# Kernel tuning notes

Hardware: AMD Instinct MI355X
Metric: run time of the kernel (lower is better)

The kernel has to match this reference:

```python
import jax, jax.numpy as jnp
import numpy as np

B, T, D = 2, 2048, 1024
H, DK, DV = 16, 64, 64
FF = 4096
EPS = 1e-6


def layer_norm(x, gamma, beta):
    mu = jnp.mean(x, axis=-1, keepdims=True)
    var = jnp.var(x, axis=-1, keepdims=True)
    return (x - mu) * jax.lax.rsqrt(var + EPS) * gamma + beta


def setup_inputs() -> dict:
    key = jax.random.key(0)
    ks = jax.random.split(key, 16)
    s = 0.02
    return {
        "inputs": jax.random.normal(ks[0], (B, T, D), jnp.float32),
        "Wq": jax.random.normal(ks[1], (D, H, DK), jnp.float32) * s,
        "Wk": jax.random.normal(ks[2], (D, H, DK), jnp.float32) * s,
        "Wv": jax.random.normal(ks[3], (D, H, DV), jnp.float32) * s,
        "Wo": jax.random.normal(ks[4], (D, H, DV), jnp.float32) * s,
        "W1": jax.random.normal(ks[5], (D, FF), jnp.float32) * s,
        "b1": jnp.zeros((FF,), jnp.float32),
        "W2": jax.random.normal(ks[6], (FF, D), jnp.float32) * s,
        "b2": jnp.zeros((D,), jnp.float32),
        "g1": jnp.ones((D,), jnp.float32),
        "be1": jnp.zeros((D,), jnp.float32),
        "g2": jnp.ones((D,), jnp.float32),
        "be2": jnp.zeros((D,), jnp.float32),
    }


def reference(inputs, Wq, Wk, Wv, Wo, W1, b1, W2, b2, g1, be1, g2, be2):
    x = inputs
    scale = 1.0 / jnp.sqrt(jnp.asarray(DK, x.dtype))
    q = jnp.einsum("btd,dhk->bthk", x, Wq) * scale
    k = jnp.einsum("bsd,dhk->bshk", x, Wk)
    v = jnp.einsum("bsd,dhv->bshv", x, Wv)
    # [B,H,T,S] attention scores; causal mask (t >= s)
    score = jnp.einsum("bshk,bthk->bhts", k, q)
    causal = jnp.tril(jnp.ones((T, T), bool))  # [T,S]
    score = jnp.where(causal[None, None], score, jnp.finfo(score.dtype).min)
    attn = jax.nn.softmax(score, axis=-1)
    ctx = jnp.einsum("bhts,bshv->bthv", attn, v)
    attn_out = jnp.einsum("bthv,dhv->btd", ctx, Wo)
    h = layer_norm(x + attn_out, g1, be1)
    ffn = jnp.maximum(h @ W1 + b1, 0.0) @ W2 + b2
    return layer_norm(h + ffn, g2, be2)
```

## Files before the change

### kernel.cpp

```cpp
#include <hip/hip_runtime.h>
#include <math.h>

#define T_SEQ 2048
#define D_MODEL 1024
#define NHEAD 16
#define DHEAD 64
#define FF_DIM 4096
#define NTOK 4096
#define LN_EPS 1e-6f

typedef unsigned short u16;
typedef __attribute__((ext_vector_type(8))) __bf16 bf16x8;
typedef __attribute__((ext_vector_type(4))) float f32x4;

typedef const void __attribute__((address_space(1))) gvoid;
typedef void __attribute__((address_space(3))) lvoid;

__device__ __forceinline__ u16 f2bf(float f) {
  unsigned u = __float_as_uint(f);
  return (u16)((u + 0x7fffu + ((u >> 16) & 1u)) >> 16);
}
__device__ __forceinline__ float bf2f(u16 u) {
  return __uint_as_float((unsigned)u << 16);
}

__device__ __forceinline__ void gll16(const u16* g, u16* l) {
  __builtin_amdgcn_global_load_lds((gvoid*)g, (lvoid*)l, 16, 0, 0);
}

__device__ __forceinline__ bf16x8 lds_frag(const u16* lds, int row, int chunk) {
  return *(const bf16x8*)&lds[row * 64 + ((chunk ^ (row & 7)) * 8)];
}

__global__ __launch_bounds__(256) void conv_f2b(const float* __restrict__ in,
                                                u16* __restrict__ out, int n) {
  const int i = (blockIdx.x * 256 + threadIdx.x) * 4;
  if (i >= n) return;
  const float4 v = *(const float4*)&in[i];
  ushort4 o;
  o.x = f2bf(v.x); o.y = f2bf(v.y); o.z = f2bf(v.z); o.w = f2bf(v.w);
  *(ushort4*)&out[i] = o;
}

__global__ __launch_bounds__(256) void transpose_f2b(
    const float* __restrict__ in, u16* __restrict__ out, int K, int N,
    float scale) {
  __shared__ u16 t[64][72];
  const int tid = threadIdx.x;
  const int k0 = blockIdx.y * 64, n0 = blockIdx.x * 64;
  const int nl = tid & 63;
#pragma unroll
  for (int i = 0; i < 16; ++i) {
    const int kl = (tid >> 6) * 16 + i;
    t[nl][kl] = f2bf(in[(size_t)(k0 + kl) * N + n0 + nl] * scale);
  }
  __syncthreads();
  const int nr = tid >> 2, kc = (tid & 3) * 16;
  const uint4 a = *(const uint4*)&t[nr][kc];
  const uint4 b = *(const uint4*)&t[nr][kc + 8];
  *(uint4*)&out[(size_t)(n0 + nr) * K + k0 + kc] = a;
  *(uint4*)&out[(size_t)(n0 + nr) * K + k0 + kc + 8] = b;
}

__global__ __launch_bounds__(256) void transpose_v(const u16* __restrict__ vin,
                                                   u16* __restrict__ vout) {
  __shared__ u16 t[64][72];
  const int tid = threadIdx.x;
  const int bh = blockIdx.y;
  const int t0 = blockIdx.x * 64;
  const u16* src = vin + ((size_t)bh * T_SEQ + t0) * 64;
#pragma unroll
  for (int i = 0; i < 2; ++i) {
    const int r = i * 32 + (tid >> 3);
    const int ch = tid & 7;
    *(uint4*)&t[r][ch * 8] = *(const uint4*)&src[(size_t)r * 64 + ch * 8];
  }
  __syncthreads();
  const int d = tid >> 2, p = (tid & 3) * 16;
  alignas(16) u16 tmp[16];
#pragma unroll
  for (int i = 0; i < 16; ++i) tmp[i] = t[p + i][d];
  u16* dst = vout + ((size_t)bh * 64 + d) * T_SEQ + t0 + p;
  *(uint4*)&dst[0] = *(const uint4*)&tmp[0];
  *(uint4*)&dst[8] = *(const uint4*)&tmp[8];
}

template <int OUTMODE, bool BIAS, bool RELU>
__global__ __launch_bounds__(256) void gemm_mfma(
    const u16* __restrict__ A, const u16* __restrict__ BT,
    const float* __restrict__ bias, void* __restrict__ C,
    int M, int N, int K, float scale) {
  __shared__ u16 smem[16384];

  const int tid = threadIdx.x;
  const int w = tid >> 6, lane = tid & 63;

  const int nwg = gridDim.x * gridDim.y;
  int bid = blockIdx.y * gridDim.x + blockIdx.x;
  const int cpx = nwg >> 3;
  bid = (bid & 7) * cpx + (bid >> 3);
  const int bx = bid % gridDim.x, by = bid / gridDim.x;
  const int m0 = by * 128, n0 = bx * 128;
  const int wr = (w >> 1) * 64, wc = (w & 1) * 64;

  f32x4 acc[4][4];
#pragma unroll
  for (int i = 0; i < 4; ++i)
#pragma unroll
    for (int j = 0; j < 4; ++j) acc[i][j] = (f32x4)0.f;

  const int srow = w * 32 + (lane >> 2);
  const int scol = (lane & 3) * 8;
  const u16* gA0 = A + (size_t)(m0 + srow) * K + scol;
  const u16* gA1 = gA0 + (size_t)16 * K;
  const u16* gB0 = BT + (size_t)(n0 + srow) * K + scol;
  const u16* gB1 = gB0 + (size_t)16 * K;

  const int arow = lane & 15;
  const int koff = (lane >> 4) * 8;

  auto stage = [&](int buf, int k0) {
    u16* base = smem + buf * 8192;
    gll16(gA0 + k0, base + w * 1024);
    gll16(gA1 + k0, base + w * 1024 + 512);
    gll16(gB0 + k0, base + 4096 + w * 1024);
    gll16(gB1 + k0, base + 4096 + w * 1024 + 512);
  };

  stage(0, 0);
  __syncthreads();

  const int nk = K >> 5;
  for (int it = 0; it < nk; ++it) {
    const int buf = it & 1;
    if (it + 1 < nk) stage(buf ^ 1, (it + 1) << 5);

    const u16* sb = smem + buf * 8192;
    bf16x8 af[4], bff[4];
#pragma unroll
    for (int m = 0; m < 4; ++m)
      af[m] = *(const bf16x8*)&sb[(wr + m * 16 + arow) * 32 + koff];
#pragma unroll
    for (int n = 0; n < 4; ++n)
      bff[n] = *(const bf16x8*)&sb[4096 + (wc + n * 16 + arow) * 32 + koff];
#pragma unroll
    for (int m = 0; m < 4; ++m)
#pragma unroll
      for (int n = 0; n < 4; ++n)
        acc[m][n] = __builtin_amdgcn_mfma_f32_16x16x32_bf16(
            af[m], bff[n], acc[m][n], 0, 0, 0);
    __syncthreads();
  }

  const int rbase = (lane >> 4) * 4;
  const int cl = lane & 15;
#pragma unroll
  for (int n = 0; n < 4; ++n) {
    const int col = n0 + wc + n * 16 + cl;
    const float bia = BIAS ? bias[col] : 0.f;
#pragma unroll
    for (int m = 0; m < 4; ++m) {
      const int row0 = m0 + wr + m * 16 + rbase;
#pragma unroll
      for (int r = 0; r < 4; ++r) {
        float vv = acc[m][n][r] * scale + bia;
        if (RELU) vv = fmaxf(vv, 0.f);
        const int row = row0 + r;
        if (OUTMODE == 1) {
          ((u16*)C)[(size_t)row * N + col] = f2bf(vv);
        } else {
          const int reg = col >> 10, cl2 = col & 1023;
          const size_t off =
              (size_t)reg * 4194304 +
              ((size_t)((row >> 11) * NHEAD + (cl2 >> 6)) * T_SEQ +
               (row & 2047)) * 64 + (cl2 & 63);
          ((u16*)C)[off] = f2bf(vv);
        }
      }
    }
  }
}

__global__ __launch_bounds__(256) void attn_mfma(
    const u16* __restrict__ qg, const u16* __restrict__ kg,
    const u16* __restrict__ vtg, u16* __restrict__ ctx) {
  __shared__ u16 Ks[2][64 * 64];
  __shared__ u16 Vs[2][64 * 64];
  __shared__ u16 Ps[4][32 * 64];

  const int tid = threadIdx.x;
  const int w = tid >> 6, lane = tid & 63;
  const int qt = gridDim.x - 1 - blockIdx.x;
  const int bh = blockIdx.y;
  const int lo = lane & 15, hi = lane >> 4;
  const int r8 = lane >> 3, cswz = (lane & 7) ^ r8;

  const u16* qhead = qg + (size_t)bh * (T_SEQ * 64);
  const u16* khead = kg + (size_t)bh * (T_SEQ * 64);
  const u16* vhead = vtg + (size_t)bh * (64 * T_SEQ);

  const int qbase = qt * 128;
  const int q0w = qbase + w * 32;
  bf16x8 qa[2][2];
#pragma unroll
  for (int u = 0; u < 2; ++u) {
    const u16* qr = &qhead[(size_t)(q0w + u * 16 + lo) * 64];
    qa[u][0] = *(const bf16x8*)&qr[hi * 8];
    qa[u][1] = *(const bf16x8*)&qr[32 + hi * 8];
  }

  f32x4 o[2][4];
#pragma unroll
  for (int u = 0; u < 2; ++u)
#pragma unroll
    for (int dt = 0; dt < 4; ++dt) o[u][dt] = (f32x4)0.f;
  float mrow[2][4], lrow[2][4];
#pragma unroll
  for (int u = 0; u < 2; ++u)
#pragma unroll
    for (int r = 0; r < 4; ++r) { mrow[u][r] = -INFINITY; lrow[u][r] = 0.f; }

  const int nt = 2 * qt + 2;

  auto stage = [&](int buf, int s0) {
#pragma unroll
    for (int i = 0; i < 2; ++i) {
      const int row = w * 16 + i * 8 + r8;
      gll16(khead + (size_t)(s0 + row) * 64 + cswz * 8,
            &Ks[buf][(w * 16 + i * 8) * 64]);
      gll16(vhead + (size_t)row * T_SEQ + s0 + cswz * 8,
            &Vs[buf][(w * 16 + i * 8) * 64]);
    }
  };

  stage(0, 0);
  __syncthreads();

  for (int it = 0; it < nt; ++it) {
    const int buf = it & 1;
    if (it + 1 < nt) stage(buf ^ 1, (it + 1) * 64);

    const bool lastT = (it == nt - 1), diagT = (it == nt - 2);
    if (!(lastT && w < 2)) {
      f32x4 s[2][4];
      __builtin_amdgcn_s_setprio(1);
#pragma unroll
      for (int c = 0; c < 4; ++c) {
        const bf16x8 kb0 = lds_frag(Ks[buf], c * 16 + lo, hi);
        const bf16x8 kb1 = lds_frag(Ks[buf], c * 16 + lo, 4 + hi);
#pragma unroll
        for (int u = 0; u < 2; ++u) {
          f32x4 a = (f32x4)0.f;
          a = __builtin_amdgcn_mfma_f32_16x16x32_bf16(qa[u][0], kb0, a, 0, 0, 0);
          a = __builtin_amdgcn_mfma_f32_16x16x32_bf16(qa[u][1], kb1, a, 0, 0, 0);
          s[u][c] = a;
        }
      }
      __builtin_amdgcn_s_setprio(0);

      if ((diagT && w < 2) || (lastT && w >= 2)) {
#pragma unroll
        for (int c = 0; c < 4; ++c) {
          const int sg = c * 16 + lo;
#pragma unroll
          for (int u = 0; u < 2; ++u)
#pragma unroll
            for (int r = 0; r < 4; ++r) {
              const int rl = (w * 32 + u * 16 + hi * 4 + r) & 63;
              if (sg > rl) s[u][c][r] = -1e30f;
            }
        }
      }

      float mx[2][4];
      bool myok = true;
#pragma unroll
      for (int u = 0; u < 2; ++u)
#pragma unroll
        for (int r = 0; r < 4; ++r) {
          float m4 = fmaxf(fmaxf(s[u][0][r], s[u][1][r]),
                           fmaxf(s[u][2][r], s[u][3][r]));
          m4 = fmaxf(m4, __shfl_xor(m4, 1));
          m4 = fmaxf(m4, __shfl_xor(m4, 2));
          m4 = fmaxf(m4, __shfl_xor(m4, 4));
          m4 = fmaxf(m4, __shfl_xor(m4, 8));
          mx[u][r] = m4;
          myok = myok && (m4 <= mrow[u][r] + 11.5f);
        }
      float corr[2][4];
#pragma unroll
      for (int u = 0; u < 2; ++u)
#pragma unroll
        for (int r = 0; r < 4; ++r) corr[u][r] = 1.f;
      if (!__all(myok)) {
#pragma unroll
        for (int u = 0; u < 2; ++u)
#pragma unroll
          for (int r = 0; r < 4; ++r) {
            const float mn = fmaxf(mrow[u][r], mx[u][r]);
            corr[u][r] = exp2f(mrow[u][r] - mn);
            mrow[u][r] = mn;
          }
#pragma unroll
        for (int u = 0; u < 2; ++u)
#pragma unroll
          for (int dt = 0; dt < 4; ++dt)
#pragma unroll
            for (int r = 0; r < 4; ++r) o[u][dt][r] *= corr[u][r];
      }
      float pr[2][4][4];
#pragma unroll
      for (int u = 0; u < 2; ++u)
#pragma unroll
        for (int r = 0; r < 4; ++r) {
          float ps = 0.f;
#pragma unroll
          for (int c = 0; c < 4; ++c) {
            pr[u][c][r] = exp2f(s[u][c][r] - mrow[u][r]);
            ps += pr[u][c][r];
          }
          ps += __shfl_xor(ps, 1);
          ps += __shfl_xor(ps, 2);
          ps += __shfl_xor(ps, 4);
          ps += __shfl_xor(ps, 8);
          lrow[u][r] = lrow[u][r] * corr[u][r] + ps;
        }

      u16* pw = &Ps[w][0];
#pragma unroll
      for (int c = 0; c < 4; ++c) {
        const int schunk = c * 2 + (lo >> 3);
        const int sb = lo & 7;
#pragma unroll
        for (int u = 0; u < 2; ++u)
#pragma unroll
          for (int r = 0; r < 4; ++r) {
            const int rw = u * 16 + hi * 4 + r;
            pw[rw * 64 + ((schunk ^ (rw & 7)) * 8) + sb] = f2bf(pr[u][c][r]);
          }
      }
      bf16x8 pa[2][2];
#pragma unroll
      for (int u = 0; u < 2; ++u) {
        pa[u][0] = lds_frag(pw, u * 16 + lo, hi);
        pa[u][1] = lds_frag(pw, u * 16 + lo, 4 + hi);
      }

      __builtin_amdgcn_s_setprio(1);
#pragma unroll
      for (int dt = 0; dt < 4; ++dt) {
        const bf16x8 vb0 = lds_frag(Vs[buf], dt * 16 + lo, hi);
        const bf16x8 vb1 = lds_frag(Vs[buf], dt * 16 + lo, 4 + hi);
#pragma unroll
        for (int u = 0; u < 2; ++u) {
          o[u][dt] = __builtin_amdgcn_mfma_f32_16x16x32_bf16(pa[u][0], vb0,
                                                             o[u][dt], 0, 0, 0);
          o[u][dt] = __builtin_amdgcn_mfma_f32_16x16x32_bf16(pa[u][1], vb1,
                                                             o[u][dt], 0, 0, 0);
        }
      }
      __builtin_amdgcn_s_setprio(0);
    }
    __syncthreads();
  }

  const int b = bh >> 4, h = bh & 15;
#pragma unroll
  for (int u = 0; u < 2; ++u)
#pragma unroll
    for (int r = 0; r < 4; ++r) {
      const float inv = 1.0f / lrow[u][r];
      const int t = qbase + w * 32 + u * 16 + hi * 4 + r;
      u16* dst = ctx + ((size_t)(b * T_SEQ + t) * NHEAD + h) * 64;
#pragma unroll
      for (int dt = 0; dt < 4; ++dt)
        dst[dt * 16 + lo] = f2bf(o[u][dt][r] * inv);
    }
}

template <bool EMIT_BF>
__global__ __launch_bounds__(256) void add_layernorm(
    const float* __restrict__ x, const u16* __restrict__ y,
    const float* __restrict__ g, const float* __restrict__ be,
    float* __restrict__ out, u16* __restrict__ out_bf) {
  const int row = blockIdx.x;
  const int tid = threadIdx.x;
  const size_t base = (size_t)row * D_MODEL + tid * 4;

  const float4 xv = *(const float4*)&x[base];
  const ushort4 yv = *(const ushort4*)&y[base];
  const float v0 = xv.x + bf2f(yv.x), v1 = xv.y + bf2f(yv.y);
  const float v2 = xv.z + bf2f(yv.z), v3 = xv.w + bf2f(yv.w);

  float s = v0 + v1 + v2 + v3;
  float ss = v0 * v0 + v1 * v1 + v2 * v2 + v3 * v3;
#pragma unroll
  for (int off = 32; off > 0; off >>= 1) {
    s += __shfl_down(s, off);
    ss += __shfl_down(ss, off);
  }
  __shared__ float red[8];
  const int wid = tid >> 6, lane = tid & 63;
  if (lane == 0) { red[wid] = s; red[4 + wid] = ss; }
  __syncthreads();
  s = red[0] + red[1] + red[2] + red[3];
  ss = red[4] + red[5] + red[6] + red[7];

  const float mean = s * (1.0f / D_MODEL);
  const float var = ss * (1.0f / D_MODEL) - mean * mean;
  const float rr = rsqrtf(var + LN_EPS);

  const float4 g4 = *(const float4*)&g[tid * 4];
  const float4 b4 = *(const float4*)&be[tid * 4];
  float4 o4;
  o4.x = (v0 - mean) * rr * g4.x + b4.x;
  o4.y = (v1 - mean) * rr * g4.y + b4.y;
  o4.z = (v2 - mean) * rr * g4.z + b4.z;
  o4.w = (v3 - mean) * rr * g4.w + b4.w;
  *(float4*)&out[base] = o4;
  if (EMIT_BF) {
    ushort4 ob;
    ob.x = f2bf(o4.x); ob.y = f2bf(o4.y); ob.z = f2bf(o4.z); ob.w = f2bf(o4.w);
    *(ushort4*)&out_bf[base] = ob;
  }
}

extern "C" void kernel_launch(void* const* d_in, const int* in_sizes, int n_in,
                              void* d_out, int out_size, void* d_ws,
                              size_t ws_size, hipStream_t stream) {
  const float* x  = (const float*)d_in[0];
  const float* Wq = (const float*)d_in[1];
  const float* Wk = (const float*)d_in[2];
  const float* Wv = (const float*)d_in[3];
  const float* Wo = (const float*)d_in[4];
  const float* W1 = (const float*)d_in[5];
  const float* b1 = (const float*)d_in[6];
  const float* W2 = (const float*)d_in[7];
  const float* b2 = (const float*)d_in[8];
  const float* g1 = (const float*)d_in[9];
  const float* be1 = (const float*)d_in[10];
  const float* g2 = (const float*)d_in[11];
  const float* be2 = (const float*)d_in[12];

  char* ws = (char*)d_ws;
  const size_t MB = 1u << 20;
  u16*   x_bf    = (u16*)(ws + 0 * MB);
  u16*   WqkvT   = (u16*)(ws + 8 * MB);
  u16*   WoB     = (u16*)(ws + 14 * MB);
  u16*   W1T     = (u16*)(ws + 16 * MB);
  u16*   W2T     = (u16*)(ws + 24 * MB);
  u16*   q_bf    = (u16*)(ws + 32 * MB);
  u16*   v_bf    = (u16*)(ws + 48 * MB);
  u16*   vT_bf   = (u16*)(ws + 56 * MB);
  u16*   ctx_bf  = (u16*)(ws + 64 * MB);
  u16*   attn_bf = (u16*)(ws + 72 * MB);
  float* h       = (float*)(ws + 80 * MB);
  u16*   h_bf    = (u16*)(ws + 0 * MB);
  u16*   ffn1_bf = (u16*)(ws + 32 * MB);
  u16*   ffn2_bf = (u16*)(ws + 8 * MB);

  const dim3 blk(256);
  const float lg2e = 1.44269504f;

  conv_f2b<<<NTOK, blk, 0, stream>>>(x, x_bf, NTOK * D_MODEL);
  transpose_f2b<<<dim3(16, 16), blk, 0, stream>>>(Wq, WqkvT, D_MODEL, D_MODEL,
                                                  0.125f * lg2e);
  transpose_f2b<<<dim3(16, 16), blk, 0, stream>>>(Wk, WqkvT + 1024 * 1024,
                                                  D_MODEL, D_MODEL, 1.f);
  transpose_f2b<<<dim3(16, 16), blk, 0, stream>>>(Wv, WqkvT + 2 * 1024 * 1024,
                                                  D_MODEL, D_MODEL, 1.f);
  conv_f2b<<<1024, blk, 0, stream>>>(Wo, WoB, D_MODEL * D_MODEL);
  transpose_f2b<<<dim3(64, 16), blk, 0, stream>>>(W1, W1T, D_MODEL, FF_DIM, 1.f);
  transpose_f2b<<<dim3(16, 64), blk, 0, stream>>>(W2, W2T, FF_DIM, D_MODEL, 1.f);

  gemm_mfma<2, false, false><<<dim3(24, 32), blk, 0, stream>>>(
      x_bf, WqkvT, nullptr, q_bf, NTOK, 3072, D_MODEL, 1.f);

  transpose_v<<<dim3(32, 32), blk, 0, stream>>>(v_bf, vT_bf);

  attn_mfma<<<dim3(T_SEQ / 128, 32), blk, 0, stream>>>(q_bf, q_bf + 4194304,
                                                       vT_bf, ctx_bf);

  gemm_mfma<1, false, false><<<dim3(8, 32), blk, 0, stream>>>(
      ctx_bf, WoB, nullptr, attn_bf, NTOK, D_MODEL, D_MODEL, 1.f);

  add_layernorm<true><<<NTOK, blk, 0, stream>>>(x, attn_bf, g1, be1, h, h_bf);

  gemm_mfma<1, true, true><<<dim3(32, 32), blk, 0, stream>>>(
      h_bf, W1T, b1, ffn1_bf, NTOK, FF_DIM, D_MODEL, 1.f);
  gemm_mfma<1, true, false><<<dim3(8, 32), blk, 0, stream>>>(
      ffn1_bf, W2T, b2, ffn2_bf, NTOK, D_MODEL, FF_DIM, 1.f);

  add_layernorm<false><<<NTOK, blk, 0, stream>>>(h, ffn2_bf, g2, be2,
                                                 (float*)d_out, nullptr);
}
```

Before: 447.0 us.

## Rewrite attention with 32x32 MFMA, transposed scores and in-register P

The attention kernel now computes S^T = K·Q^T with 32x32x16 MFMAs, so each lane owns one query row. Row max and sum then need only one cross-half shuffle, and the softmax state is a single scalar per lane. P is packed to bf16 with v_cvt_pk_bf16_f32 and rearranged with v_permlane32_swap, so it feeds the PV MFMA directly and the LDS round-trip for P is gone. The output goes through an LDS staging buffer (reusing Ks) so the context store is coalesced in 16-byte writes. The cost is larger accumulator register footprint and inline asm that ties the kernel to gfx950 instructions.

```diff
diff --git a/kernel.cpp b/kernel.cpp
--- a/kernel.cpp
+++ b/kernel.cpp
@@ -10,8 +10,10 @@
 #define LN_EPS 1e-6f
 
 typedef unsigned short u16;
+typedef unsigned int u32;
 typedef __attribute__((ext_vector_type(8))) __bf16 bf16x8;
 typedef __attribute__((ext_vector_type(4))) float f32x4;
+typedef __attribute__((ext_vector_type(16))) float f32x16;
 
 typedef const void __attribute__((address_space(1))) gvoid;
 typedef void __attribute__((address_space(3))) lvoid;
@@ -23,6 +25,11 @@
 __device__ __forceinline__ float bf2f(u16 u) {
   return __uint_as_float((unsigned)u << 16);
 }
+__device__ __forceinline__ u32 cvtpk(float lo, float hi) {
+  u32 r;
+  asm("v_cvt_pk_bf16_f32 %0, %1, %2" : "=v"(r) : "v"(lo), "v"(hi));
+  return r;
+}
 
 __device__ __forceinline__ void gll16(const u16* g, u16* l) {
   __builtin_amdgcn_global_load_lds((gvoid*)g, (lvoid*)l, 16, 0, 0);
@@ -31,6 +38,8 @@
 __device__ __forceinline__ bf16x8 lds_frag(const u16* lds, int row, int chunk) {
   return *(const bf16x8*)&lds[row * 64 + ((chunk ^ (row & 7)) * 8)];
 }
+
+union BF8 { u32 u[4]; bf16x8 v; };
 
 __global__ __launch_bounds__(256) void conv_f2b(const float* __restrict__ in,
                                                 u16* __restrict__ out, int n) {
@@ -186,13 +195,12 @@
     const u16* __restrict__ vtg, u16* __restrict__ ctx) {
   __shared__ u16 Ks[2][64 * 64];
   __shared__ u16 Vs[2][64 * 64];
-  __shared__ u16 Ps[4][32 * 64];
 
   const int tid = threadIdx.x;
   const int w = tid >> 6, lane = tid & 63;
   const int qt = gridDim.x - 1 - blockIdx.x;
   const int bh = blockIdx.y;
-  const int lo = lane & 15, hi = lane >> 4;
+  const int l31 = lane & 31, hi32 = lane >> 5;
   const int r8 = lane >> 3, cswz = (lane & 7) ^ r8;
 
   const u16* qhead = qg + (size_t)bh * (T_SEQ * 64);
@@ -200,25 +208,15 @@
   const u16* vhead = vtg + (size_t)bh * (64 * T_SEQ);
 
   const int qbase = qt * 128;
-  const int q0w = qbase + w * 32;
-  bf16x8 qa[2][2];
-#pragma unroll
-  for (int u = 0; u < 2; ++u) {
-    const u16* qr = &qhead[(size_t)(q0w + u * 16 + lo) * 64];
-    qa[u][0] = *(const bf16x8*)&qr[hi * 8];
-    qa[u][1] = *(const bf16x8*)&qr[32 + hi * 8];
-  }
-
-  f32x4 o[2][4];
-#pragma unroll
-  for (int u = 0; u < 2; ++u)
-#pragma unroll
-    for (int dt = 0; dt < 4; ++dt) o[u][dt] = (f32x4)0.f;
-  float mrow[2][4], lrow[2][4];
-#pragma unroll
-  for (int u = 0; u < 2; ++u)
-#pragma unroll
-    for (int r = 0; r < 4; ++r) { mrow[u][r] = -INFINITY; lrow[u][r] = 0.f; }
+  const int qrow = qbase + w * 32 + l31;
+
+  bf16x8 qb[4];
+#pragma unroll
+  for (int ks2 = 0; ks2 < 4; ++ks2)
+    qb[ks2] = *(const bf16x8*)&qhead[(size_t)qrow * 64 + ks2 * 16 + hi32 * 8];
+
+  f32x16 o0 = (f32x16)0.f, o1 = (f32x16)0.f;
+  float m = -INFINITY, l = 0.f;
 
   const int nt = 2 * qt + 2;
 
@@ -242,140 +240,125 @@
 
     const bool lastT = (it == nt - 1), diagT = (it == nt - 2);
     if (!(lastT && w < 2)) {
-      f32x4 s[2][4];
+      f32x16 st0 = (f32x16)0.f, st1 = (f32x16)0.f;
       __builtin_amdgcn_s_setprio(1);
 #pragma unroll
-      for (int c = 0; c < 4; ++c) {
-        const bf16x8 kb0 = lds_frag(Ks[buf], c * 16 + lo, hi);
-        const bf16x8 kb1 = lds_frag(Ks[buf], c * 16 + lo, 4 + hi);
-#pragma unroll
-        for (int u = 0; u < 2; ++u) {
-          f32x4 a = (f32x4)0.f;
-          a = __builtin_amdgcn_mfma_f32_16x16x32_bf16(qa[u][0], kb0, a, 0, 0, 0);
-          a = __builtin_amdgcn_mfma_f32_16x16x32_bf16(qa[u][1], kb1, a, 0, 0, 0);
-          s[u][c] = a;
+      for (int ks2 = 0; ks2 < 4; ++ks2) {
+        const bf16x8 kf0 = lds_frag(Ks[buf], l31, ks2 * 2 + hi32);
+        st0 = __builtin_amdgcn_mfma_f32_32x32x16_bf16(kf0, qb[ks2], st0, 0, 0, 0);
+      }
+#pragma unroll
+      for (int ks2 = 0; ks2 < 4; ++ks2) {
+        const bf16x8 kf1 = lds_frag(Ks[buf], 32 + l31, ks2 * 2 + hi32);
+        st1 = __builtin_amdgcn_mfma_f32_32x32x16_bf16(kf1, qb[ks2], st1, 0, 0, 0);
+      }
+      __builtin_amdgcn_s_setprio(0);
+
+      if ((diagT && w < 2) || (lastT && w >= 2)) {
+        const int s0g = it * 64;
+#pragma unroll
+        for (int r = 0; r < 16; ++r) {
+          const int rowm = (r & 3) + 8 * (r >> 2) + 4 * hi32;
+          if (s0g + rowm > qrow) st0[r] = -1e30f;
+          if (s0g + 32 + rowm > qrow) st1[r] = -1e30f;
         }
       }
-      __builtin_amdgcn_s_setprio(0);
-
-      if ((diagT && w < 2) || (lastT && w >= 2)) {
-#pragma unroll
-        for (int c = 0; c < 4; ++c) {
-          const int sg = c * 16 + lo;
-#pragma unroll
-          for (int u = 0; u < 2; ++u)
-#pragma unroll
-            for (int r = 0; r < 4; ++r) {
-              const int rl = (w * 32 + u * 16 + hi * 4 + r) & 63;
-              if (sg > rl) s[u][c][r] = -1e30f;
-            }
+
+      float mx = fmaxf(st0[0], st1[0]);
+#pragma unroll
+      for (int r = 1; r < 16; ++r) mx = fmaxf(mx, fmaxf(st0[r], st1[r]));
+      mx = fmaxf(mx, __shfl_xor(mx, 32));
+
+      float corr = 1.f;
+      if (!__all(mx <= m + 11.5f)) {
+        const float mn = fmaxf(m, mx);
+        corr = exp2f(m - mn);
+        m = mn;
+#pragma unroll
+        for (int r = 0; r < 16; ++r) { o0[r] *= corr; o1[r] *= corr; }
+      }
+      float ps = 0.f;
+#pragma unroll
+      for (int r = 0; r < 16; ++r) {
+        st0[r] = exp2f(st0[r] - m);
+        st1[r] = exp2f(st1[r] - m);
+        ps += st0[r] + st1[r];
+      }
+      ps += __shfl_xor(ps, 32);
+      l = l * corr + ps;
+
+      BF8 pb[4];
+#pragma unroll
+      for (int blk = 0; blk < 2; ++blk) {
+        {
+          u32 x0 = cvtpk(st0[blk * 8 + 0], st0[blk * 8 + 1]);
+          u32 x1 = cvtpk(st0[blk * 8 + 2], st0[blk * 8 + 3]);
+          u32 y0 = cvtpk(st0[blk * 8 + 4], st0[blk * 8 + 5]);
+          u32 y1 = cvtpk(st0[blk * 8 + 6], st0[blk * 8 + 7]);
+          asm("v_permlane32_swap_b32 %0, %1" : "+v"(x0), "+v"(y0));
+          asm("v_permlane32_swap_b32 %0, %1" : "+v"(x1), "+v"(y1));
+          pb[blk].u[0] = x0; pb[blk].u[1] = x1;
+          pb[blk].u[2] = y0; pb[blk].u[3] = y1;
         }
-      }
-
-      float mx[2][4];
-      bool myok = true;
-#pragma unroll
-      for (int u = 0; u < 2; ++u)
-#pragma unroll
-        for (int r = 0; r < 4; ++r) {
-          float m4 = fmaxf(fmaxf(s[u][0][r], s[u][1][r]),
-                           fmaxf(s[u][2][r], s[u][3][r]));
-          m4 = fmaxf(m4, __shfl_xor(m4, 1));
-          m4 = fmaxf(m4, __shfl_xor(m4, 2));
-          m4 = fmaxf(m4, __shfl_xor(m4, 4));
-          m4 = fmaxf(m4, __shfl_xor(m4, 8));
-          mx[u][r] = m4;
-          myok = myok && (m4 <= mrow[u][r] + 11.5f);
+        {
+          u32 x0 = cvtpk(st1[blk * 8 + 0], st1[blk * 8 + 1]);
+          u32 x1 = cvtpk(st1[blk * 8 + 2], st1[blk * 8 + 3]);
+          u32 y0 = cvtpk(st1[blk * 8 + 4], st1[blk * 8 + 5]);
+          u32 y1 = cvtpk(st1[blk * 8 + 6], st1[blk * 8 + 7]);
+          asm("v_permlane32_swap_b32 %0, %1" : "+v"(x0), "+v"(y0));
+          asm("v_permlane32_swap_b32 %0, %1" : "+v"(x1), "+v"(y1));
+          pb[2 + blk].u[0] = x0; pb[2 + blk].u[1] = x1;
+          pb[2 + blk].u[2] = y0; pb[2 + blk].u[3] = y1;
         }
-      float corr[2][4];
-#pragma unroll
-      for (int u = 0; u < 2; ++u)
-#pragma unroll
-        for (int r = 0; r < 4; ++r) corr[u][r] = 1.f;
-      if (!__all(myok)) {
-#pragma unroll
-        for (int u = 0; u < 2; ++u)
-#pragma unroll
-          for (int r = 0; r < 4; ++r) {
-            const float mn = fmaxf(mrow[u][r], mx[u][r]);
-            corr[u][r] = exp2f(mrow[u][r] - mn);
-            mrow[u][r] = mn;
-          }
-#pragma unroll
-        for (int u = 0; u < 2; ++u)
-#pragma unroll
-          for (int dt = 0; dt < 4; ++dt)
-#pragma unroll
-            for (int r = 0; r < 4; ++r) o[u][dt][r] *= corr[u][r];
-      }
-      float pr[2][4][4];
-#pragma unroll
-      for (int u = 0; u < 2; ++u)
-#pragma unroll
-        for (int r = 0; r < 4; ++r) {
-          float ps = 0.f;
-#pragma unroll
-          for (int c = 0; c < 4; ++c) {
-            pr[u][c][r] = exp2f(s[u][c][r] - mrow[u][r]);
-            ps += pr[u][c][r];
-          }
-          ps += __shfl_xor(ps, 1);
-          ps += __shfl_xor(ps, 2);
-          ps += __shfl_xor(ps, 4);
-          ps += __shfl_xor(ps, 8);
-          lrow[u][r] = lrow[u][r] * corr[u][r] + ps;
-        }
-
-      u16* pw = &Ps[w][0];
-#pragma unroll
-      for (int c = 0; c < 4; ++c) {
-        const int schunk = c * 2 + (lo >> 3);
-        const int sb = lo & 7;
-#pragma unroll
-        for (int u = 0; u < 2; ++u)
-#pragma unroll
-          for (int r = 0; r < 4; ++r) {
-            const int rw = u * 16 + hi * 4 + r;
-            pw[rw * 64 + ((schunk ^ (rw & 7)) * 8) + sb] = f2bf(pr[u][c][r]);
-          }
-      }
-      bf16x8 pa[2][2];
-#pragma unroll
-      for (int u = 0; u < 2; ++u) {
-        pa[u][0] = lds_frag(pw, u * 16 + lo, hi);
-        pa[u][1] = lds_frag(pw, u * 16 + lo, 4 + hi);
       }
 
       __builtin_amdgcn_s_setprio(1);
 #pragma unroll
-      for (int dt = 0; dt < 4; ++dt) {
-        const bf16x8 vb0 = lds_frag(Vs[buf], dt * 16 + lo, hi);
-        const bf16x8 vb1 = lds_frag(Vs[buf], dt * 16 + lo, 4 + hi);
-#pragma unroll
-        for (int u = 0; u < 2; ++u) {
-          o[u][dt] = __builtin_amdgcn_mfma_f32_16x16x32_bf16(pa[u][0], vb0,
-                                                             o[u][dt], 0, 0, 0);
-          o[u][dt] = __builtin_amdgcn_mfma_f32_16x16x32_bf16(pa[u][1], vb1,
-                                                             o[u][dt], 0, 0, 0);
-        }
+      for (int ks = 0; ks < 4; ++ks) {
+        const bf16x8 vf0 = lds_frag(Vs[buf], l31, ks * 2 + hi32);
+        o0 = __builtin_amdgcn_mfma_f32_32x32x16_bf16(vf0, pb[ks].v, o0, 0, 0, 0);
+      }
+#pragma unroll
+      for (int ks = 0; ks < 4; ++ks) {
+        const bf16x8 vf1 = lds_frag(Vs[buf], 32 + l31, ks * 2 + hi32);
+        o1 = __builtin_amdgcn_mfma_f32_32x32x16_bf16(vf1, pb[ks].v, o1, 0, 0, 0);
       }
       __builtin_amdgcn_s_setprio(0);
     }
     __syncthreads();
   }
 
+  const float inv = 1.0f / l;
+#pragma unroll
+  for (int r = 0; r < 16; ++r) { o0[r] *= inv; o1[r] *= inv; }
+
+  u16* ep = &Ks[0][0] + w * 2048;
+#pragma unroll
+  for (int rg = 0; rg < 4; ++rg) {
+    const u32 w0 = cvtpk(o0[rg * 4 + 0], o0[rg * 4 + 1]);
+    const u32 w1 = cvtpk(o0[rg * 4 + 2], o0[rg * 4 + 3]);
+    uint2 val; val.x = w0; val.y = w1;
+    *(uint2*)&ep[l31 * 64 + ((rg ^ (l31 & 7)) * 8) + hi32 * 4] = val;
+  }
+#pragma unroll
+  for (int rg = 0; rg < 4; ++rg) {
+    const u32 w0 = cvtpk(o1[rg * 4 + 0], o1[rg * 4 + 1]);
+    const u32 w1 = cvtpk(o1[rg * 4 + 2], o1[rg * 4 + 3]);
+    const int chunk = 4 + rg;
+    uint2 val; val.x = w0; val.y = w1;
+    *(uint2*)&ep[l31 * 64 + ((chunk ^ (l31 & 7)) * 8) + hi32 * 4] = val;
+  }
+
   const int b = bh >> 4, h = bh & 15;
-#pragma unroll
-  for (int u = 0; u < 2; ++u)
-#pragma unroll
-    for (int r = 0; r < 4; ++r) {
-      const float inv = 1.0f / lrow[u][r];
-      const int t = qbase + w * 32 + u * 16 + hi * 4 + r;
-      u16* dst = ctx + ((size_t)(b * T_SEQ + t) * NHEAD + h) * 64;
-#pragma unroll
-      for (int dt = 0; dt < 4; ++dt)
-        dst[dt * 16 + lo] = f2bf(o[u][dt][r] * inv);
-    }
+  const int ql = lane >> 1, half = lane & 1;
+  const int t = qbase + w * 32 + ql;
+  u16* dst = ctx + ((size_t)(b * T_SEQ + t) * NHEAD + h) * 64;
+#pragma unroll
+  for (int j = 0; j < 4; ++j) {
+    const int chunk = half * 4 + j;
+    const uint4 vv = *(const uint4*)&ep[ql * 64 + ((chunk ^ (ql & 7)) * 8)];
+    *(uint4*)&dst[chunk * 8] = vv;
+  }
 }
 
 template <bool EMIT_BF>
```

Measured after the change: 401.4 us. -10.2%, faster.
